# Kernel optimization log

Hardware: AMD Instinct MI355X
Metric: run time of the kernel (lower is better)

## Reference

```python
import jax, jax.numpy as jnp
import numpy as np

N_NODES = 100000

def setup_inputs() -> dict:
    key = jax.random.key(0)
    k1, k2, k3, k4, k5, k6 = jax.random.split(key, 6)
    n_edges = 3200000
    edge_rows = jnp.sort(jax.random.randint(k1, (n_edges,), 0, N_NODES))
    edge_cols = jax.random.randint(k2, (n_edges,), 0, N_NODES)
    edge_vals = jax.random.uniform(k3, (n_edges,), dtype=jnp.float32)
    h = jax.random.normal(k4, (N_NODES, 128), dtype=jnp.float32)
    W = jax.random.normal(k5, (128, 128), dtype=jnp.float32) * (1.0 / np.sqrt(128))
    b = jax.random.normal(k6, (128,), dtype=jnp.float32) * 0.01
    return {"edge_rows": edge_rows, "edge_cols": edge_cols, "edge_vals": edge_vals,
            "h": h, "W": W, "b": b}

def reference(edge_rows, edge_cols, edge_vals, h, W, b):
    # SpMM: out[i] = sum over edges e with row[e]==i of vals[e] * h[col[e]]
    msgs = edge_vals[:, None] * h[edge_cols]            # [E, d]
    agg = jax.ops.segment_sum(msgs, edge_rows, num_segments=N_NODES)  # [N, d]
    # Linear + activation (nn.Linear: x @ W.T + b)
    out = agg @ W.T + b
    return jax.nn.relu(out)
```

## Files before the change

### kernel.cpp

```cpp
#include <hip/hip_runtime.h>

#define N_NODES 100000
#define D 128

typedef unsigned short ushort_t;
typedef __attribute__((ext_vector_type(8))) short short8;
typedef __attribute__((ext_vector_type(4))) float f32x4;

__device__ __forceinline__ unsigned f2bf(float x) {
    unsigned u = __float_as_uint(x);
    return (u + 0x7fffu + ((u >> 16) & 1u)) >> 16;
}

__global__ __launch_bounds__(64)
void build_wfrag_kernel(const float* __restrict__ W,
                        ushort_t* __restrict__ Wfrag) {
    const int t  = blockIdx.x;
    const int jt = t >> 2, kt = t & 3;
    const int l  = threadIdx.x;
    const float* src = W + (size_t)(jt * 16 + (l & 15)) * D + kt * 32 + (l >> 4) * 8;
    const float4 p0 = *reinterpret_cast<const float4*>(src);
    const float4 p1 = *reinterpret_cast<const float4*>(src + 4);
    uint4 o;
    o.x = f2bf(p0.x) | (f2bf(p0.y) << 16);
    o.y = f2bf(p0.z) | (f2bf(p0.w) << 16);
    o.z = f2bf(p1.x) | (f2bf(p1.y) << 16);
    o.w = f2bf(p1.z) | (f2bf(p1.w) << 16);
    *reinterpret_cast<uint4*>(Wfrag + ((size_t)t * 64 + l) * 8) = o;
}

__global__ void build_rowptr_kernel(const int* __restrict__ rows,
                                    int* __restrict__ row_ptr, int n_edges) {
    int i = blockIdx.x * blockDim.x + threadIdx.x;
    if (i > N_NODES) return;
    int lo = 0, hi = n_edges;
    while (lo < hi) {
        int mid = (lo + hi) >> 1;
        if (rows[mid] < i) lo = mid + 1; else hi = mid;
    }
    row_ptr[i] = lo;
}

__global__ __launch_bounds__(256)
void gemm_G_kernel(const float* __restrict__ h,
                   const ushort_t* __restrict__ Wfrag,
                   ushort_t* __restrict__ G) {
    const int wave = threadIdx.x >> 6;
    const int l    = threadIdx.x & 63;
    const int tile = blockIdx.x * 4 + wave;
    if (tile >= N_NODES / 16) return;
    const int n0   = tile * 16;
    const int lrow = l & 15;
    const int lk   = l >> 4;

    union { short8 v; ushort_t u[8]; } bfrag[4];
    const float* hp = h + (size_t)(n0 + lrow) * D + lk * 8;
#pragma unroll
    for (int kt = 0; kt < 4; ++kt) {
        const float4 q0 = *reinterpret_cast<const float4*>(hp + kt * 32);
        const float4 q1 = *reinterpret_cast<const float4*>(hp + kt * 32 + 4);
        bfrag[kt].u[0] = (ushort_t)f2bf(q0.x);
        bfrag[kt].u[1] = (ushort_t)f2bf(q0.y);
        bfrag[kt].u[2] = (ushort_t)f2bf(q0.z);
        bfrag[kt].u[3] = (ushort_t)f2bf(q0.w);
        bfrag[kt].u[4] = (ushort_t)f2bf(q1.x);
        bfrag[kt].u[5] = (ushort_t)f2bf(q1.y);
        bfrag[kt].u[6] = (ushort_t)f2bf(q1.z);
        bfrag[kt].u[7] = (ushort_t)f2bf(q1.w);
    }

    const uint4* wf = reinterpret_cast<const uint4*>(Wfrag) + l;
#pragma unroll
    for (int jt = 0; jt < 8; ++jt) {
        f32x4 acc = {0.f, 0.f, 0.f, 0.f};
#pragma unroll
        for (int kt = 0; kt < 4; ++kt) {
            union { uint4 q; short8 v; } af;
            af.q = wf[(jt * 4 + kt) * 64];
            acc = __builtin_amdgcn_mfma_f32_16x16x32_bf16(af.v, bfrag[kt].v,
                                                          acc, 0, 0, 0);
        }
        uint2 o;
        o.x = f2bf(acc[0]) | (f2bf(acc[1]) << 16);
        o.y = f2bf(acc[2]) | (f2bf(acc[3]) << 16);
        *reinterpret_cast<uint2*>(G + (size_t)(n0 + lrow) * D + jt * 16 + lk * 4) = o;
    }
}

__device__ __forceinline__ void acc8(float2& a0, float2& a1, float2& a2,
                                     float2& a3, float v, uint4 g) {
    a0.x += v * __uint_as_float(g.x << 16);
    a0.y += v * __uint_as_float(g.x & 0xffff0000u);
    a1.x += v * __uint_as_float(g.y << 16);
    a1.y += v * __uint_as_float(g.y & 0xffff0000u);
    a2.x += v * __uint_as_float(g.z << 16);
    a2.y += v * __uint_as_float(g.z & 0xffff0000u);
    a3.x += v * __uint_as_float(g.w << 16);
    a3.y += v * __uint_as_float(g.w & 0xffff0000u);
}

__global__ __launch_bounds__(256)
void gconv_gather_kernel(const int* __restrict__ cols,
                         const float* __restrict__ vals,
                         const ushort_t* __restrict__ G,
                         const float* __restrict__ b,
                         const int* __restrict__ row_ptr,
                         float* __restrict__ out) {
    const int tid  = blockIdx.x * 256 + threadIdx.x;
    const int node = tid >> 4;
    const int il   = tid & 15;

    int e = row_ptr[node];
    const int end = row_ptr[node + 1];
    const ushort_t* gp = G + il * 8;

    float2 a0 = make_float2(0.f, 0.f), a1 = make_float2(0.f, 0.f);
    float2 a2 = make_float2(0.f, 0.f), a3 = make_float2(0.f, 0.f);

    for (; e + 3 < end; e += 4) {
        const int c0 = cols[e];
        const int c1 = cols[e + 1];
        const int c2 = cols[e + 2];
        const int c3 = cols[e + 3];
        const float v0 = vals[e];
        const float v1 = vals[e + 1];
        const float v2 = vals[e + 2];
        const float v3 = vals[e + 3];
        const uint4 g0 = *reinterpret_cast<const uint4*>(gp + (size_t)c0 * D);
        const uint4 g1 = *reinterpret_cast<const uint4*>(gp + (size_t)c1 * D);
        const uint4 g2 = *reinterpret_cast<const uint4*>(gp + (size_t)c2 * D);
        const uint4 g3 = *reinterpret_cast<const uint4*>(gp + (size_t)c3 * D);
        acc8(a0, a1, a2, a3, v0, g0);
        acc8(a0, a1, a2, a3, v1, g1);
        acc8(a0, a1, a2, a3, v2, g2);
        acc8(a0, a1, a2, a3, v3, g3);
    }
    for (; e < end; ++e) {
        const int   c = cols[e];
        const float v = vals[e];
        const uint4 g = *reinterpret_cast<const uint4*>(gp + (size_t)c * D);
        acc8(a0, a1, a2, a3, v, g);
    }

    const float4 b0 = *reinterpret_cast<const float4*>(b + il * 8);
    const float4 b1 = *reinterpret_cast<const float4*>(b + il * 8 + 4);
    float4 r0, r1;
    r0.x = a0.x + b0.x; r0.y = a0.y + b0.y;
    r0.z = a1.x + b0.z; r0.w = a1.y + b0.w;
    r1.x = a2.x + b1.x; r1.y = a2.y + b1.y;
    r1.z = a3.x + b1.z; r1.w = a3.y + b1.w;
    r0.x = r0.x > 0.f ? r0.x : 0.f;
    r0.y = r0.y > 0.f ? r0.y : 0.f;
    r0.z = r0.z > 0.f ? r0.z : 0.f;
    r0.w = r0.w > 0.f ? r0.w : 0.f;
    r1.x = r1.x > 0.f ? r1.x : 0.f;
    r1.y = r1.y > 0.f ? r1.y : 0.f;
    r1.z = r1.z > 0.f ? r1.z : 0.f;
    r1.w = r1.w > 0.f ? r1.w : 0.f;
    float* op = out + (size_t)node * D + il * 8;
    *reinterpret_cast<float4*>(op)     = r0;
    *reinterpret_cast<float4*>(op + 4) = r1;
}

extern "C" void kernel_launch(void* const* d_in, const int* in_sizes, int n_in,
                              void* d_out, int out_size, void* d_ws,
                              size_t ws_size, hipStream_t stream) {
    const int*   edge_rows = (const int*)d_in[0];
    const int*   edge_cols = (const int*)d_in[1];
    const float* edge_vals = (const float*)d_in[2];
    const float* h         = (const float*)d_in[3];
    const float* W         = (const float*)d_in[4];
    const float* b         = (const float*)d_in[5];
    float*       out       = (float*)d_out;

    const int n_edges = in_sizes[0];

    ushort_t* Wfrag   = (ushort_t*)d_ws;
    int*      row_ptr = (int*)((char*)d_ws + 64 * 1024);
    ushort_t* G       = (ushort_t*)((char*)d_ws + 64 * 1024 + 512 * 1024);

    build_wfrag_kernel<<<32, 64, 0, stream>>>(W, Wfrag);

    const int rp_threads = 256;
    const int rp_blocks  = (N_NODES + 1 + rp_threads - 1) / rp_threads;
    build_rowptr_kernel<<<rp_blocks, rp_threads, 0, stream>>>(edge_rows,
                                                              row_ptr, n_edges);

    const int n_tiles = N_NODES / 16;
    gemm_G_kernel<<<(n_tiles + 3) / 4, 256, 0, stream>>>(h, Wfrag, G);

    gconv_gather_kernel<<<N_NODES * 16 / 256, 256, 0, stream>>>(
        edge_cols, edge_vals, G, b, row_ptr, out);
}
```

Before: 153.2 us.

## Quantize projected features to int8, degree-sort nodes, and build rowptr from edge boundaries

The projected feature table is now stored as per-row-scaled uint8 with an offset instead of bf16, halving the bytes the random gather reads per edge. Nodes are reordered by degree through a histogram, scan and scatter so waves handle similarly sized rows. The row-pointer build switches from a per-node binary search to per-edge boundary detection, and the gather uses vectorized nontemporal loads of cols and vals unrolled by eight. This adds several small kernel launches and lowers precision to 8 bits, which risks exceeding the accuracy tolerance.

```diff
diff --git a/kernel.cpp b/kernel.cpp
--- a/kernel.cpp
+++ b/kernel.cpp
@@ -4,8 +4,10 @@
 #define D 128
 
 typedef unsigned short ushort_t;
+typedef unsigned char uchar_t;
 typedef __attribute__((ext_vector_type(8))) short short8;
 typedef __attribute__((ext_vector_type(4))) float f32x4;
+typedef __attribute__((ext_vector_type(4))) int i32x4;
 
 __device__ __forceinline__ unsigned f2bf(float x) {
     unsigned u = __float_as_uint(x);
@@ -29,22 +31,69 @@
     *reinterpret_cast<uint4*>(Wfrag + ((size_t)t * 64 + l) * 8) = o;
 }
 
-__global__ void build_rowptr_kernel(const int* __restrict__ rows,
-                                    int* __restrict__ row_ptr, int n_edges) {
-    int i = blockIdx.x * blockDim.x + threadIdx.x;
-    if (i > N_NODES) return;
-    int lo = 0, hi = n_edges;
-    while (lo < hi) {
-        int mid = (lo + hi) >> 1;
-        if (rows[mid] < i) lo = mid + 1; else hi = mid;
-    }
-    row_ptr[i] = lo;
-}
-
-__global__ __launch_bounds__(256)
-void gemm_G_kernel(const float* __restrict__ h,
-                   const ushort_t* __restrict__ Wfrag,
-                   ushort_t* __restrict__ G) {
+__global__ __launch_bounds__(256)
+void build_rowptr_boundary_kernel(const int* __restrict__ rows,
+                                  int* __restrict__ row_ptr, int n_edges) {
+    const int e = blockIdx.x * 256 + threadIdx.x;
+    if (e >= n_edges) return;
+    const int r0 = rows[e];
+    if (e == 0) {
+        for (int r = 0; r <= r0; ++r) row_ptr[r] = 0;
+    }
+    if (e + 1 < n_edges) {
+        const int r1 = rows[e + 1];
+        for (int r = r0 + 1; r <= r1; ++r) row_ptr[r] = e + 1;
+    } else {
+        for (int r = r0 + 1; r <= N_NODES; ++r) row_ptr[r] = n_edges;
+    }
+}
+
+__global__ void hist_zero_kernel(int* __restrict__ hist) {
+    hist[threadIdx.x] = 0;
+}
+
+__global__ __launch_bounds__(256)
+void degree_hist_kernel(const int* __restrict__ row_ptr,
+                        int* __restrict__ hist) {
+    const int i = blockIdx.x * 256 + threadIdx.x;
+    if (i >= N_NODES) return;
+    int deg = row_ptr[i + 1] - row_ptr[i];
+    deg = deg > 255 ? 255 : deg;
+    atomicAdd(&hist[deg], 1);
+}
+
+__global__ __launch_bounds__(256)
+void scan_hist_kernel(const int* __restrict__ hist, int* __restrict__ offs) {
+    __shared__ int tmp[256];
+    const int t = threadIdx.x;
+    tmp[t] = hist[t];
+    __syncthreads();
+#pragma unroll
+    for (int d = 1; d < 256; d <<= 1) {
+        int v = (t >= d) ? tmp[t - d] : 0;
+        __syncthreads();
+        tmp[t] += v;
+        __syncthreads();
+    }
+    offs[t] = (t == 0) ? 0 : tmp[t - 1];
+}
+
+__global__ __launch_bounds__(256)
+void scatter_perm_kernel(const int* __restrict__ row_ptr,
+                         int* __restrict__ offs, int* __restrict__ perm) {
+    const int i = blockIdx.x * 256 + threadIdx.x;
+    if (i >= N_NODES) return;
+    int deg = row_ptr[i + 1] - row_ptr[i];
+    deg = deg > 255 ? 255 : deg;
+    const int slot = atomicAdd(&offs[deg], 1);
+    perm[slot] = i;
+}
+
+__global__ __launch_bounds__(256)
+void gemm_Gq_kernel(const float* __restrict__ h,
+                    const ushort_t* __restrict__ Wfrag,
+                    uchar_t* __restrict__ Gq,
+                    float* __restrict__ scales) {
     const int wave = threadIdx.x >> 6;
     const int l    = threadIdx.x & 63;
     const int tile = blockIdx.x * 4 + wave;
@@ -70,96 +119,128 @@
     }
 
     const uint4* wf = reinterpret_cast<const uint4*>(Wfrag) + l;
+    f32x4 acc[8];
 #pragma unroll
     for (int jt = 0; jt < 8; ++jt) {
-        f32x4 acc = {0.f, 0.f, 0.f, 0.f};
+        acc[jt] = (f32x4){0.f, 0.f, 0.f, 0.f};
 #pragma unroll
         for (int kt = 0; kt < 4; ++kt) {
             union { uint4 q; short8 v; } af;
             af.q = wf[(jt * 4 + kt) * 64];
-            acc = __builtin_amdgcn_mfma_f32_16x16x32_bf16(af.v, bfrag[kt].v,
-                                                          acc, 0, 0, 0);
+            acc[jt] = __builtin_amdgcn_mfma_f32_16x16x32_bf16(
+                af.v, bfrag[kt].v, acc[jt], 0, 0, 0);
         }
-        uint2 o;
-        o.x = f2bf(acc[0]) | (f2bf(acc[1]) << 16);
-        o.y = f2bf(acc[2]) | (f2bf(acc[3]) << 16);
-        *reinterpret_cast<uint2*>(G + (size_t)(n0 + lrow) * D + jt * 16 + lk * 4) = o;
-    }
-}
-
-__device__ __forceinline__ void acc8(float2& a0, float2& a1, float2& a2,
-                                     float2& a3, float v, uint4 g) {
-    a0.x += v * __uint_as_float(g.x << 16);
-    a0.y += v * __uint_as_float(g.x & 0xffff0000u);
-    a1.x += v * __uint_as_float(g.y << 16);
-    a1.y += v * __uint_as_float(g.y & 0xffff0000u);
-    a2.x += v * __uint_as_float(g.z << 16);
-    a2.y += v * __uint_as_float(g.z & 0xffff0000u);
-    a3.x += v * __uint_as_float(g.w << 16);
-    a3.y += v * __uint_as_float(g.w & 0xffff0000u);
-}
-
-__global__ __launch_bounds__(256)
-void gconv_gather_kernel(const int* __restrict__ cols,
-                         const float* __restrict__ vals,
-                         const ushort_t* __restrict__ G,
-                         const float* __restrict__ b,
-                         const int* __restrict__ row_ptr,
-                         float* __restrict__ out) {
+    }
+
+    float amax = 0.f;
+#pragma unroll
+    for (int jt = 0; jt < 8; ++jt) {
+#pragma unroll
+        for (int r = 0; r < 4; ++r) amax = fmaxf(amax, fabsf(acc[jt][r]));
+    }
+    amax = fmaxf(amax, __shfl_xor(amax, 16));
+    amax = fmaxf(amax, __shfl_xor(amax, 32));
+    const float s   = amax > 0.f ? amax * (1.f / 127.f) : 1.f;
+    const float inv = amax > 0.f ? 127.f / amax : 0.f;
+
+#pragma unroll
+    for (int jt = 0; jt < 8; ++jt) {
+        const unsigned q0 = (unsigned)((int)rintf(acc[jt][0] * inv) + 128);
+        const unsigned q1 = (unsigned)((int)rintf(acc[jt][1] * inv) + 128);
+        const unsigned q2 = (unsigned)((int)rintf(acc[jt][2] * inv) + 128);
+        const unsigned q3 = (unsigned)((int)rintf(acc[jt][3] * inv) + 128);
+        const unsigned pk = q0 | (q1 << 8) | (q2 << 16) | (q3 << 24);
+        *reinterpret_cast<unsigned*>(
+            Gq + (size_t)(n0 + lrow) * D + jt * 16 + lk * 4) = pk;
+    }
+    if (l < 16) scales[n0 + l] = s;
+}
+
+__device__ __forceinline__ void accq(float* a, float& vsum, float vs, uint2 g) {
+    a[0] += vs * (float)(g.x & 0xffu);
+    a[1] += vs * (float)((g.x >> 8) & 0xffu);
+    a[2] += vs * (float)((g.x >> 16) & 0xffu);
+    a[3] += vs * (float)(g.x >> 24);
+    a[4] += vs * (float)(g.y & 0xffu);
+    a[5] += vs * (float)((g.y >> 8) & 0xffu);
+    a[6] += vs * (float)((g.y >> 16) & 0xffu);
+    a[7] += vs * (float)(g.y >> 24);
+    vsum += vs;
+}
+
+__global__ __launch_bounds__(256)
+void gconv_gather_q2_kernel(const int* __restrict__ cols,
+                            const float* __restrict__ vals,
+                            const uchar_t* __restrict__ Gq,
+                            const float* __restrict__ scales,
+                            const float* __restrict__ bias,
+                            const int* __restrict__ row_ptr,
+                            const int* __restrict__ perm,
+                            float* __restrict__ out) {
     const int tid  = blockIdx.x * 256 + threadIdx.x;
-    const int node = tid >> 4;
     const int il   = tid & 15;
+    const int node = perm[tid >> 4];
 
     int e = row_ptr[node];
     const int end = row_ptr[node + 1];
-    const ushort_t* gp = G + il * 8;
-
-    float2 a0 = make_float2(0.f, 0.f), a1 = make_float2(0.f, 0.f);
-    float2 a2 = make_float2(0.f, 0.f), a3 = make_float2(0.f, 0.f);
-
-    for (; e + 3 < end; e += 4) {
-        const int c0 = cols[e];
-        const int c1 = cols[e + 1];
-        const int c2 = cols[e + 2];
-        const int c3 = cols[e + 3];
-        const float v0 = vals[e];
-        const float v1 = vals[e + 1];
-        const float v2 = vals[e + 2];
-        const float v3 = vals[e + 3];
-        const uint4 g0 = *reinterpret_cast<const uint4*>(gp + (size_t)c0 * D);
-        const uint4 g1 = *reinterpret_cast<const uint4*>(gp + (size_t)c1 * D);
-        const uint4 g2 = *reinterpret_cast<const uint4*>(gp + (size_t)c2 * D);
-        const uint4 g3 = *reinterpret_cast<const uint4*>(gp + (size_t)c3 * D);
-        acc8(a0, a1, a2, a3, v0, g0);
-        acc8(a0, a1, a2, a3, v1, g1);
-        acc8(a0, a1, a2, a3, v2, g2);
-        acc8(a0, a1, a2, a3, v3, g3);
+    const uchar_t* gp = Gq + il * 8;
+
+    float a[8];
+#pragma unroll
+    for (int j = 0; j < 8; ++j) a[j] = 0.f;
+    float vsum = 0.f;
+
+    while (e < end && (e & 3)) {
+        const int c = cols[e];
+        const float vs = vals[e] * scales[c];
+        const uint2 g = *reinterpret_cast<const uint2*>(gp + (size_t)c * D);
+        accq(a, vsum, vs, g);
+        ++e;
+    }
+    for (; e + 7 < end; e += 8) {
+        const i32x4 ca = __builtin_nontemporal_load(
+            reinterpret_cast<const i32x4*>(cols + e));
+        const i32x4 cb = __builtin_nontemporal_load(
+            reinterpret_cast<const i32x4*>(cols + e + 4));
+        const f32x4 va = __builtin_nontemporal_load(
+            reinterpret_cast<const f32x4*>(vals + e));
+        const f32x4 vb = __builtin_nontemporal_load(
+            reinterpret_cast<const f32x4*>(vals + e + 4));
+        const int c[8] = {ca[0], ca[1], ca[2], ca[3], cb[0], cb[1], cb[2], cb[3]};
+        const float v[8] = {va[0], va[1], va[2], va[3], vb[0], vb[1], vb[2], vb[3]};
+        float s[8];
+#pragma unroll
+        for (int i = 0; i < 8; ++i) s[i] = scales[c[i]];
+        uint2 g[8];
+#pragma unroll
+        for (int i = 0; i < 8; ++i)
+            g[i] = *reinterpret_cast<const uint2*>(gp + (size_t)c[i] * D);
+#pragma unroll
+        for (int i = 0; i < 8; ++i) accq(a, vsum, v[i] * s[i], g[i]);
     }
     for (; e < end; ++e) {
-        const int   c = cols[e];
-        const float v = vals[e];
-        const uint4 g = *reinterpret_cast<const uint4*>(gp + (size_t)c * D);
-        acc8(a0, a1, a2, a3, v, g);
-    }
-
-    const float4 b0 = *reinterpret_cast<const float4*>(b + il * 8);
-    const float4 b1 = *reinterpret_cast<const float4*>(b + il * 8 + 4);
-    float4 r0, r1;
-    r0.x = a0.x + b0.x; r0.y = a0.y + b0.y;
-    r0.z = a1.x + b0.z; r0.w = a1.y + b0.w;
-    r1.x = a2.x + b1.x; r1.y = a2.y + b1.y;
-    r1.z = a3.x + b1.z; r1.w = a3.y + b1.w;
-    r0.x = r0.x > 0.f ? r0.x : 0.f;
-    r0.y = r0.y > 0.f ? r0.y : 0.f;
-    r0.z = r0.z > 0.f ? r0.z : 0.f;
-    r0.w = r0.w > 0.f ? r0.w : 0.f;
-    r1.x = r1.x > 0.f ? r1.x : 0.f;
-    r1.y = r1.y > 0.f ? r1.y : 0.f;
-    r1.z = r1.z > 0.f ? r1.z : 0.f;
-    r1.w = r1.w > 0.f ? r1.w : 0.f;
+        const int c = cols[e];
+        const float vs = vals[e] * scales[c];
+        const uint2 g = *reinterpret_cast<const uint2*>(gp + (size_t)c * D);
+        accq(a, vsum, vs, g);
+    }
+
+    const float4 b0 = *reinterpret_cast<const float4*>(bias + il * 8);
+    const float4 b1 = *reinterpret_cast<const float4*>(bias + il * 8 + 4);
+    const float corr = 128.f * vsum;
+    f32x4 r0, r1;
+    r0[0] = a[0] - corr + b0.x; r0[1] = a[1] - corr + b0.y;
+    r0[2] = a[2] - corr + b0.z; r0[3] = a[3] - corr + b0.w;
+    r1[0] = a[4] - corr + b1.x; r1[1] = a[5] - corr + b1.y;
+    r1[2] = a[6] - corr + b1.z; r1[3] = a[7] - corr + b1.w;
+#pragma unroll
+    for (int i = 0; i < 4; ++i) {
+        r0[i] = r0[i] > 0.f ? r0[i] : 0.f;
+        r1[i] = r1[i] > 0.f ? r1[i] : 0.f;
+    }
     float* op = out + (size_t)node * D + il * 8;
-    *reinterpret_cast<float4*>(op)     = r0;
-    *reinterpret_cast<float4*>(op + 4) = r1;
+    __builtin_nontemporal_store(r0, reinterpret_cast<f32x4*>(op));
+    __builtin_nontemporal_store(r1, reinterpret_cast<f32x4*>(op + 4));
 }
 
 extern "C" void kernel_launch(void* const* d_in, const int* in_sizes, int n_in,
@@ -175,20 +256,37 @@
 
     const int n_edges = in_sizes[0];
 
+    const size_t OFF_RP   = 64 * 1024;
+    const size_t OFF_SC   = OFF_RP + 512 * 1024;
+    const size_t OFF_PERM = OFF_SC + 512 * 1024;
+    const size_t OFF_HIST = OFF_PERM + 512 * 1024;
+    const size_t OFF_OFFS = OFF_HIST + 4 * 1024;
+    const size_t OFF_GQ   = OFF_OFFS + 4 * 1024;
+
     ushort_t* Wfrag   = (ushort_t*)d_ws;
-    int*      row_ptr = (int*)((char*)d_ws + 64 * 1024);
-    ushort_t* G       = (ushort_t*)((char*)d_ws + 64 * 1024 + 512 * 1024);
+    int*      row_ptr = (int*)((char*)d_ws + OFF_RP);
+    float*    scales  = (float*)((char*)d_ws + OFF_SC);
+    int*      perm    = (int*)((char*)d_ws + OFF_PERM);
+    int*      hist    = (int*)((char*)d_ws + OFF_HIST);
+    int*      offs    = (int*)((char*)d_ws + OFF_OFFS);
+    uchar_t*  Gq      = (uchar_t*)((char*)d_ws + OFF_GQ);
 
     build_wfrag_kernel<<<32, 64, 0, stream>>>(W, Wfrag);
 
-    const int rp_threads = 256;
-    const int rp_blocks  = (N_NODES + 1 + rp_threads - 1) / rp_threads;
-    build_rowptr_kernel<<<rp_blocks, rp_threads, 0, stream>>>(edge_rows,
-                                                              row_ptr, n_edges);
-
-    const int n_tiles = N_NODES / 16;
-    gemm_G_kernel<<<(n_tiles + 3) / 4, 256, 0, stream>>>(h, Wfrag, G);
-
-    gconv_gather_kernel<<<N_NODES * 16 / 256, 256, 0, stream>>>(
-        edge_cols, edge_vals, G, b, row_ptr, out);
-}
+    build_rowptr_boundary_kernel<<<(n_edges + 255) / 256, 256, 0, stream>>>(
+        edge_rows, row_ptr, n_edges);
+
+    const int nb_nodes = (N_NODES + 255) / 256;
+    hist_zero_kernel<<<1, 256, 0, stream>>>(hist);
+    degree_hist_kernel<<<nb_nodes, 256, 0, stream>>>(row_ptr, hist);
+    scan_hist_kernel<<<1, 256, 0, stream>>>(hist, offs);
+    scatter_perm_kernel<<<nb_nodes, 256, 0, stream>>>(row_ptr, offs, perm);
+
+    const int n_tiles     = N_NODES / 16;
+    const int gemm_blocks = (n_tiles + 3) / 4;
+    gemm_Gq_kernel<<<gemm_blocks, 256, 0, stream>>>(h, Wfrag, Gq, scales);
+
+    const int gather_blocks = N_NODES * 16 / 256;
+    gconv_gather_q2_kernel<<<gather_blocks, 256, 0, stream>>>(
+        edge_cols, edge_vals, Gq, scales, b, row_ptr, perm, out);
+}
```

After: 505.7 us. 3.3x slower.
